# Optimization experiments

Measured on AMD Instinct MI355X. Metric: run time of the kernel, lower is better.

Reference implementation:

```python
import jax, jax.numpy as jnp
from jax import lax
import numpy as np

B, L, M, D, K, STRIDE = 32, 32768, 32, 128, 16, 8


def setup_inputs() -> dict:
    key = jax.random.key(0)
    k1, k2, k3, k4 = jax.random.split(key, 4)
    x = jax.random.normal(k1, (B, L, M), dtype=jnp.float32)
    # sorted timestamps per sample, like torch.sort(rand*100)
    timestamps = jnp.sort(jax.random.uniform(k2, (B, L), dtype=jnp.float32) * 100.0, axis=1)
    fan_in = M * K
    bound = 1.0 / np.sqrt(fan_in)
    conv_w = jax.random.uniform(k3, (D, M, K), dtype=jnp.float32, minval=-bound, maxval=bound)
    conv_b = jax.random.uniform(k4, (D,), dtype=jnp.float32, minval=-bound, maxval=bound)
    return {"x": x, "timestamps": timestamps, "conv_w": conv_w, "conv_b": conv_b}


def reference(x, timestamps, conv_w, conv_b):
    # Conv1d patch embedding: x [B,L,M] -> NCL -> conv -> [B,P,D]
    patches = lax.conv_general_dilated(
        x.transpose(0, 2, 1), conv_w,
        window_strides=(STRIDE,), padding=[(0, 0)],
        dimension_numbers=("NCH", "OIH", "NCH"))
    patches = patches.transpose(0, 2, 1) + conv_b  # [B,P,D]
    P = patches.shape[1]

    # Per-patch median timestamp (padding=0 -> all windows full length K).
    # torch.median on even-length returns the LOWER median = sorted idx (K-1)//2.
    starts = jnp.arange(P) * STRIDE
    idx = starts[:, None] + jnp.arange(K)          # [P,K]
    windows = timestamps[:, idx]                   # [B,P,K]
    med = jnp.sort(windows, axis=-1)[..., (K - 1) // 2]  # [B,P]

    # Sinusoidal PE at continuous times.
    div_term = jnp.exp(jnp.arange(0, D, 2).astype(jnp.float32) * (-np.log(10000.0) / D))
    ang = med[..., None] * div_term                # [B,P,D//2]
    pe = jnp.stack([jnp.sin(ang), jnp.cos(ang)], axis=-1).reshape(med.shape[0], P, D)
    return patches + pe
```

## Files before the change

### kernel.cpp

```cpp
#include <hip/hip_runtime.h>
#include <hip/hip_bf16.h>

#define Bn 32
#define Ln 32768
#define Mn 32
#define Dn 128
#define Pn 4095
#define KKn 512

typedef short  bf16x8 __attribute__((ext_vector_type(8)));
typedef float  f32x4  __attribute__((ext_vector_type(4)));
typedef __attribute__((address_space(3))) unsigned int       lds_u32;
typedef const __attribute__((address_space(1))) unsigned int glb_u32;

union BU { bf16x8 v; unsigned short u[8]; };

static __device__ __forceinline__ unsigned short f2bf(float f) {
  __hip_bfloat16 h = __float2bfloat16(f);
  return *reinterpret_cast<unsigned short*>(&h);
}

static __device__ __forceinline__ bf16x8 cvt8(const f32x4& a, const f32x4& b) {
  BU bu;
  bu.u[0] = f2bf(a[0]); bu.u[1] = f2bf(a[1]); bu.u[2] = f2bf(a[2]); bu.u[3] = f2bf(a[3]);
  bu.u[4] = f2bf(b[0]); bu.u[5] = f2bf(b[1]); bu.u[6] = f2bf(b[2]); bu.u[7] = f2bf(b[3]);
  return bu.v;
}

static __device__ __forceinline__ int phi(int g) {
  return g ^ ((g >> 6) & 7);
}

__global__ __launch_bounds__(256) void prep_w_kernel(const float* __restrict__ w,
                                                     unsigned short* __restrict__ wswz) {
  int idx = blockIdx.x * 256 + threadIdx.x;
  int j = idx & 7;
  int d = (idx >> 3) & 127;
  int g = idx >> 10;
  int kk = g * 8 + j;
  int k = kk >> 5;
  int m = kk & 31;
  wswz[idx] = f2bf(w[(d << 9) + (m << 4) + k]);
}

__global__ __launch_bounds__(256, 4) void gemm_pe_kernel(
    const float* __restrict__ x,
    const float* __restrict__ ts,
    const unsigned short* __restrict__ wswz,
    const float* __restrict__ bias,
    float* __restrict__ out) {

  __shared__ float xsf[9216];
  __shared__ float tsl[32];

  const int b    = blockIdx.y;
  const int tile = blockIdx.x;
  const int tid  = threadIdx.x;
  const int lane = tid & 63;
  const int wv   = tid >> 6;
  const int mrow = lane & 15;
  const int quad = lane >> 4;

  if (tid < 32)
    tsl[tid] = ts[(size_t)b * Ln + tile * 256 + tid * 8 + 7];

  {
    const size_t slab0g = (((size_t)b * Ln * Mn) >> 2) + (size_t)tile * 2048;
    const size_t xg_max = (((size_t)Bn * Ln * Mn) >> 2) - 1;
    #pragma unroll
    for (int j = 0; j < 9; ++j) {
      const int Pw = wv * 576 + j * 64;
      const int P  = Pw + lane;
      size_t gg = slab0g + (size_t)phi(P);
      if (gg > xg_max) gg = xg_max;
      __builtin_amdgcn_global_load_lds((glb_u32*)(x + (gg << 2)),
                                       (lds_u32*)&xsf[(size_t)Pw << 2], 16, 0, 0);
    }
  }

  const unsigned short* bq = wswz + (((quad << 7) + (wv << 5) + mrow) << 3);
  bf16x8 bp[3][2];
  #pragma unroll
  for (int j = 0; j < 3; ++j) {
    bp[j][0] = *reinterpret_cast<const bf16x8*>(bq + j * 4096);
    bp[j][1] = *reinterpret_cast<const bf16x8*>(bq + j * 4096 + 128);
  }

  __syncthreads();

  int agbase[2];
  #pragma unroll
  for (int pt = 0; pt < 2; ++pt) agbase[pt] = (pt * 16 + mrow) * 64 + quad * 2;

  f32x4 acc[2][2] = {};

  #pragma unroll
  for (int t = 0; t < 16; ++t) {
    const int cur = t % 3;
    bf16x8 af[2];
    #pragma unroll
    for (int pt = 0; pt < 2; ++pt) {
      const int G  = agbase[pt] + t * 8;
      const int gl = phi(G);
      const int gh = gl ^ 1;
      f32x4 lo = *reinterpret_cast<const f32x4*>(&xsf[gl * 4]);
      f32x4 hi = *reinterpret_cast<const f32x4*>(&xsf[gh * 4]);
      af[pt] = cvt8(lo, hi);
    }
    bf16x8 bc0 = bp[cur][0], bc1 = bp[cur][1];
    if (t < 13) {
      bp[cur][0] = *reinterpret_cast<const bf16x8*>(bq + (t + 3) * 4096);
      bp[cur][1] = *reinterpret_cast<const bf16x8*>(bq + (t + 3) * 4096 + 128);
    }
    #pragma unroll
    for (int pt = 0; pt < 2; ++pt) {
      acc[pt][0] = __builtin_amdgcn_mfma_f32_16x16x32_bf16(af[pt], bc0, acc[pt][0], 0, 0, 0);
      acc[pt][1] = __builtin_amdgcn_mfma_f32_16x16x32_bf16(af[pt], bc1, acc[pt][1], 0, 0, 0);
    }
  }

  const int d0 = wv * 32 + mrow;
  const float NEG_C = -0.14391156831212810f;
  const float div0  = __expf(NEG_C * (float)(d0 >> 1));
  const float div1  = __expf(NEG_C * (float)((d0 + 16) >> 1));
  const float phs   = (d0 & 1) ? 1.5707963267948966f : 0.0f;
  const float bias0 = bias[d0];
  const float bias1 = bias[d0 + 16];

  #pragma unroll
  for (int pt = 0; pt < 2; ++pt) {
    const int plbase = pt * 16 + quad * 4;
    f32x4 med4 = *reinterpret_cast<const f32x4*>(&tsl[plbase]);
    const int pbase = tile * 32 + plbase;
    float* ob = out + ((size_t)b * Pn + pbase) * Dn + d0;
    #pragma unroll
    for (int reg = 0; reg < 4; ++reg) {
      if (pbase + reg < Pn) {
        float m = med4[reg];
        float pe0 = __sinf(m * div0 + phs);
        float pe1 = __sinf(m * div1 + phs);
        ob[reg * Dn]      = acc[pt][0][reg] + bias0 + pe0;
        ob[reg * Dn + 16] = acc[pt][1][reg] + bias1 + pe1;
      }
    }
  }
}

extern "C" void kernel_launch(void* const* d_in, const int* in_sizes, int n_in,
                              void* d_out, int out_size, void* d_ws, size_t ws_size,
                              hipStream_t stream) {
  const float* x      = (const float*)d_in[0];
  const float* ts     = (const float*)d_in[1];
  const float* conv_w = (const float*)d_in[2];
  const float* conv_b = (const float*)d_in[3];
  float* out = (float*)d_out;
  unsigned short* wswz = (unsigned short*)d_ws;

  prep_w_kernel<<<256, 256, 0, stream>>>(conv_w, wswz);
  gemm_pe_kernel<<<dim3(128, Bn), 256, 0, stream>>>(x, ts, wswz, conv_b, out);
}
```

Before: 229.2 us.

## Stage x tile in LDS as bf16 via register loads instead of fp32 async copy

Replaces the direct global-to-LDS fp32 copy with register loads that convert to bf16 once before writing LDS, halving LDS footprint and removing per-MFMA-step conversion work. The swizzle is adjusted for the new 16-byte bf16 rows, occupancy hint raised to 8 blocks, and the B-operand prefetch depth cut from 3 to 2 to save registers. In exchange the loads are no longer asynchronous into LDS, so global latency passes through registers and the conversion happens in a serialized two-phase staging.

```diff
diff --git a/kernel.cpp b/kernel.cpp
--- a/kernel.cpp
+++ b/kernel.cpp
@@ -9,26 +9,22 @@
 #define KKn 512
 
 typedef short  bf16x8 __attribute__((ext_vector_type(8)));
+typedef short  bf16x4 __attribute__((ext_vector_type(4)));
 typedef float  f32x4  __attribute__((ext_vector_type(4)));
-typedef __attribute__((address_space(3))) unsigned int       lds_u32;
-typedef const __attribute__((address_space(1))) unsigned int glb_u32;
-
-union BU { bf16x8 v; unsigned short u[8]; };
 
 static __device__ __forceinline__ unsigned short f2bf(float f) {
   __hip_bfloat16 h = __float2bfloat16(f);
   return *reinterpret_cast<unsigned short*>(&h);
 }
 
-static __device__ __forceinline__ bf16x8 cvt8(const f32x4& a, const f32x4& b) {
-  BU bu;
-  bu.u[0] = f2bf(a[0]); bu.u[1] = f2bf(a[1]); bu.u[2] = f2bf(a[2]); bu.u[3] = f2bf(a[3]);
-  bu.u[4] = f2bf(b[0]); bu.u[5] = f2bf(b[1]); bu.u[6] = f2bf(b[2]); bu.u[7] = f2bf(b[3]);
+static __device__ __forceinline__ bf16x4 cvt4(const float4& a) {
+  union { bf16x4 v; unsigned short u[4]; } bu;
+  bu.u[0] = f2bf(a.x); bu.u[1] = f2bf(a.y); bu.u[2] = f2bf(a.z); bu.u[3] = f2bf(a.w);
   return bu.v;
 }
 
 static __device__ __forceinline__ int phi(int g) {
-  return g ^ ((g >> 6) & 7);
+  return g ^ ((g >> 5) & 7);
 }
 
 __global__ __launch_bounds__(256) void prep_w_kernel(const float* __restrict__ w,
@@ -43,14 +39,14 @@
   wswz[idx] = f2bf(w[(d << 9) + (m << 4) + k]);
 }
 
-__global__ __launch_bounds__(256, 4) void gemm_pe_kernel(
+__global__ __launch_bounds__(256, 8) void gemm_pe_kernel(
     const float* __restrict__ x,
     const float* __restrict__ ts,
     const unsigned short* __restrict__ wswz,
     const float* __restrict__ bias,
     float* __restrict__ out) {
 
-  __shared__ float xsf[9216];
+  __shared__ unsigned short xs[1056 * 8];
   __shared__ float tsl[32];
 
   const int b    = blockIdx.y;
@@ -61,27 +57,53 @@
   const int mrow = lane & 15;
   const int quad = lane >> 4;
 
-  if (tid < 32)
-    tsl[tid] = ts[(size_t)b * Ln + tile * 256 + tid * 8 + 7];
+  const size_t slab0g = (((size_t)b * Ln * Mn) >> 2) + (size_t)tile * 2048;
+  const float* xg0 = x + (slab0g << 2);
 
-  {
-    const size_t slab0g = (((size_t)b * Ln * Mn) >> 2) + (size_t)tile * 2048;
-    const size_t xg_max = (((size_t)Bn * Ln * Mn) >> 2) - 1;
-    #pragma unroll
-    for (int j = 0; j < 9; ++j) {
-      const int Pw = wv * 576 + j * 64;
-      const int P  = Pw + lane;
-      size_t gg = slab0g + (size_t)phi(P);
-      if (gg > xg_max) gg = xg_max;
-      __builtin_amdgcn_global_load_lds((glb_u32*)(x + (gg << 2)),
-                                       (lds_u32*)&xsf[(size_t)Pw << 2], 16, 0, 0);
-    }
+  float4 fA[4];
+  #pragma unroll
+  for (int j = 0; j < 4; ++j)
+    fA[j] = *reinterpret_cast<const float4*>(xg0 + (((size_t)j * 256 + tid) << 2));
+  __builtin_amdgcn_sched_barrier(0);
+  #pragma unroll
+  for (int j = 0; j < 4; ++j) {
+    int G = j * 256 + tid;
+    int o = G >> 1, h = G & 1;
+    *reinterpret_cast<bf16x4*>(&xs[phi(o) * 8 + h * 4]) = cvt4(fA[j]);
   }
 
+  float4 fB[4];
+  #pragma unroll
+  for (int j = 0; j < 4; ++j)
+    fB[j] = *reinterpret_cast<const float4*>(xg0 + (((size_t)(j + 4) * 256 + tid) << 2));
+  float4 ft = make_float4(0.f, 0.f, 0.f, 0.f);
+  if (tid < 64) {
+    size_t gg = slab0g + 2048 + tid;
+    const size_t xg_max = (((size_t)Bn * Ln * Mn) >> 2) - 1;
+    if (gg > xg_max) gg = xg_max;
+    ft = *reinterpret_cast<const float4*>(x + (gg << 2));
+  }
+  float tsv = 0.f;
+  if (tid < 32)
+    tsv = ts[(size_t)b * Ln + tile * 256 + tid * 8 + 7];
+  __builtin_amdgcn_sched_barrier(0);
+  #pragma unroll
+  for (int j = 0; j < 4; ++j) {
+    int G = (j + 4) * 256 + tid;
+    int o = G >> 1, h = G & 1;
+    *reinterpret_cast<bf16x4*>(&xs[phi(o) * 8 + h * 4]) = cvt4(fB[j]);
+  }
+  if (tid < 64) {
+    int G = 2048 + tid;
+    int o = G >> 1, h = G & 1;
+    *reinterpret_cast<bf16x4*>(&xs[phi(o) * 8 + h * 4]) = cvt4(ft);
+  }
+  if (tid < 32) tsl[tid] = tsv;
+
   const unsigned short* bq = wswz + (((quad << 7) + (wv << 5) + mrow) << 3);
-  bf16x8 bp[3][2];
+  bf16x8 bp[2][2];
   #pragma unroll
-  for (int j = 0; j < 3; ++j) {
+  for (int j = 0; j < 2; ++j) {
     bp[j][0] = *reinterpret_cast<const bf16x8*>(bq + j * 4096);
     bp[j][1] = *reinterpret_cast<const bf16x8*>(bq + j * 4096 + 128);
   }
@@ -90,27 +112,21 @@
 
   int agbase[2];
   #pragma unroll
-  for (int pt = 0; pt < 2; ++pt) agbase[pt] = (pt * 16 + mrow) * 64 + quad * 2;
+  for (int pt = 0; pt < 2; ++pt) agbase[pt] = (pt * 16 + mrow) * 32 + quad;
 
   f32x4 acc[2][2] = {};
 
   #pragma unroll
   for (int t = 0; t < 16; ++t) {
-    const int cur = t % 3;
+    const int cur = t & 1;
     bf16x8 af[2];
     #pragma unroll
-    for (int pt = 0; pt < 2; ++pt) {
-      const int G  = agbase[pt] + t * 8;
-      const int gl = phi(G);
-      const int gh = gl ^ 1;
-      f32x4 lo = *reinterpret_cast<const f32x4*>(&xsf[gl * 4]);
-      f32x4 hi = *reinterpret_cast<const f32x4*>(&xsf[gh * 4]);
-      af[pt] = cvt8(lo, hi);
-    }
+    for (int pt = 0; pt < 2; ++pt)
+      af[pt] = *reinterpret_cast<const bf16x8*>(&xs[phi(agbase[pt] + t * 4) * 8]);
     bf16x8 bc0 = bp[cur][0], bc1 = bp[cur][1];
-    if (t < 13) {
-      bp[cur][0] = *reinterpret_cast<const bf16x8*>(bq + (t + 3) * 4096);
-      bp[cur][1] = *reinterpret_cast<const bf16x8*>(bq + (t + 3) * 4096 + 128);
+    if (t < 14) {
+      bp[cur][0] = *reinterpret_cast<const bf16x8*>(bq + (t + 2) * 4096);
+      bp[cur][1] = *reinterpret_cast<const bf16x8*>(bq + (t + 2) * 4096 + 128);
     }
     #pragma unroll
     for (int pt = 0; pt < 2; ++pt) {
```

New measurement: 231.4 us. Within noise of the previous version (+1.0%).
